# Kernel tuning notes

Hardware: AMD Instinct MI355X
Metric: run time of the kernel (lower is better)

## Reference

```python
import jax, jax.numpy as jnp
import numpy as np

B, C, H, W = 16, 256, 64, 64
NH, DH = 8, 64
POS_C = 4


def setup_inputs() -> dict:
    key = jax.random.key(0)
    ks = jax.random.split(key, 10)
    cin = C + POS_C
    dqkv = NH * DH
    sc = 1.0 / np.sqrt(cin)
    inp = {
        "x": jax.random.normal(ks[0], (B, C, H, W), dtype=jnp.float32),
        "pos_emb": jax.random.normal(ks[1], (1, POS_C, H, W), dtype=jnp.float32) / np.sqrt(C * H * W),
        "Wk": jax.random.normal(ks[2], (dqkv, cin), dtype=jnp.float32) * sc,
        "bk": jnp.zeros((dqkv,), dtype=jnp.float32),
        "Wq": jax.random.normal(ks[3], (dqkv, cin), dtype=jnp.float32) * sc,
        "bq": jnp.zeros((dqkv,), dtype=jnp.float32),
        "Wv": jax.random.normal(ks[4], (dqkv, cin), dtype=jnp.float32) * sc,
        "bv": jnp.zeros((dqkv,), dtype=jnp.float32),
        "Wo": jax.random.normal(ks[5], (C, dqkv), dtype=jnp.float32) / np.sqrt(dqkv),
        "bo": jnp.zeros((C,), dtype=jnp.float32),
    }
    return inp


def _conv1x1(w, b, x):
    # w: (out, in), x: (B, in, H, W) -> (B, out, H, W)
    return jnp.einsum('oc,bchw->bohw', w, x) + b[None, :, None, None]


def reference(x, pos_emb, Wk, bk, Wq, bq, Wv, bv, Wo, bo):
    b, c, h, w = x.shape
    xp = jnp.concatenate([x, jnp.broadcast_to(pos_emb, (b, POS_C, h, w))], axis=1)
    K = _conv1x1(Wk, bk, xp).reshape(b, NH, DH, h, w)
    Q = _conv1x1(Wq, bq, xp).reshape(b, NH, DH, h, w)
    V = _conv1x1(Wv, bv, xp).reshape(b, NH, DH, h, w)
    # Row (width-axis) logits: (B, nh, H, W, W)
    qk_w = jnp.einsum('bhdij,bhdik->bhijk', Q, K)
    # Column (height-axis) logits: (B, nh, H, W, H)
    qk_h = jnp.einsum('bhdij,bhdkj->bhijk', Q, K)
    scale = 1.0 / np.sqrt(w + h)
    p = jax.nn.softmax(jnp.concatenate([qk_w, qk_h], axis=-1) * scale, axis=-1)
    p_w, p_h = p[..., :w], p[..., w:]
    a_w = jnp.einsum('bhijk,bhdik->bhdij', p_w, V)
    a_h = jnp.einsum('bhijk,bhdkj->bhdij', p_h, V)
    A = (a_w + a_h).reshape(b, NH * DH, h, w)
    return x + _conv1x1(Wo, bo, A)
```

## Files before the change

kernel.cpp:

```cpp
#include <hip/hip_runtime.h>

typedef unsigned short u16;
typedef __bf16 bf16x8 __attribute__((ext_vector_type(8)));
typedef float f32x4 __attribute__((ext_vector_type(4)));
typedef unsigned short u16x8 __attribute__((ext_vector_type(8)));
typedef unsigned short u16x4 __attribute__((ext_vector_type(4)));

#define MFMA16(A,B,C) __builtin_amdgcn_mfma_f32_16x16x32_bf16(A,B,C,0,0,0)

__device__ __forceinline__ float b2f(u16 h){ unsigned u = ((unsigned)h)<<16; return __builtin_bit_cast(float,u); }
__device__ __forceinline__ u16 f2b(float f){ unsigned u = __builtin_bit_cast(unsigned,f); u += 0x7fffu + ((u>>16)&1u); return (u16)(u>>16); }
__device__ __forceinline__ bf16x8 ldb8(const u16* p){ return __builtin_bit_cast(bf16x8, *(const u16x8*)p); }

__device__ __forceinline__ void g2lds16(const u16* g, u16* l){
  __builtin_amdgcn_global_load_lds((const __attribute__((address_space(1))) void*)g,
                                   (__attribute__((address_space(3))) void*)l, 16, 0, 0);
}

#define BAR   __builtin_amdgcn_s_barrier()
#define LGKM0 do{ asm volatile("s_waitcnt lgkmcnt(0)" ::: "memory"); __builtin_amdgcn_sched_barrier(0); }while(0)
#define VMC4  asm volatile("s_waitcnt vmcnt(4)" ::: "memory")
#define VMC0  asm volatile("s_waitcnt vmcnt(0)" ::: "memory")


__global__ void k_prep_w(const float* __restrict__ Wq, const float* __restrict__ Wk,
                         const float* __restrict__ Wv, const float* __restrict__ bq,
                         const float* __restrict__ bk, const float* __restrict__ bv,
                         const float* __restrict__ Wo,
                         u16* __restrict__ WP, u16* __restrict__ BIAS,
                         u16* __restrict__ WoP){
  int r = blockIdx.x;
  int tid = threadIdx.x;
  if (r < 1536){
    int t = r >> 9, rm = r & 511;
    const float* src = (t==0 ? Wq : (t==1 ? Wk : Wv)) + (long)rm*260;
    WP[(long)r*320 + tid] = f2b(src[tid]);
    if (tid < 64) WP[(long)r*320 + 256 + tid] = (tid < 4) ? f2b(src[256 + tid]) : (u16)0;
    if (tid == 0){
      const float* bs = (t==0 ? bq : (t==1 ? bk : bv));
      BIAS[r] = f2b(bs[rm]);
    }
  } else {
    int co = r - 1536;
    WoP[(long)co*512 + tid]       = f2b(Wo[(long)co*512 + tid]);
    WoP[(long)co*512 + 256 + tid] = f2b(Wo[(long)co*512 + 256 + tid]);
  }
}

__global__ void k_sentinel(float* __restrict__ out){
  long i = (long)blockIdx.x*256 + threadIdx.x;
  out[i] = 100.0f;
}

__global__ __launch_bounds__(256) void k_cvtx(const float* __restrict__ x,
                                              const float* __restrict__ pos,
                                              u16* __restrict__ XT, int b0){
  __shared__ u16 tile[64*65];
  int bidx = blockIdx.x;
  int ct = bidx & 3, pt = (bidx>>2)&63, bl = bidx>>8;
  int c0 = ct*64, p0 = pt*64;
  int tid = threadIdx.x;
  const float* xb = x + (long)(b0+bl)*256*4096;
  #pragma unroll
  for (int it=0; it<16; ++it){
    int idx = it*256 + tid; int cc = idx>>6, px = idx&63;
    tile[cc*65 + px] = f2b(xb[(long)(c0+cc)*4096 + p0 + px]);
  }
  __syncthreads();
  u16* dst = XT + ((long)(bl*4096 + p0))*320 + c0;
  #pragma unroll
  for (int it=0; it<4; ++it){
    int idx = it*256 + tid; int pp = idx>>4, c4 = (idx&15)*4;
    u16x4 o;
    #pragma unroll
    for (int u=0;u<4;++u) o[u] = tile[(c4+u)*65 + pp];
    *(u16x4*)&dst[(long)pp*320 + c4] = o;
  }
  if (ct == 0){
    int px = tid>>2, cb = (tid&3)*16;
    u16* row = XT + ((long)(bl*4096 + p0 + px))*320 + 256 + cb;
    #pragma unroll
    for (int half=0; half<2; ++half){
      u16x8 o;
      #pragma unroll
      for (int u=0;u<8;++u){
        int c = cb + half*8 + u;
        o[u] = (c < 4) ? f2b(pos[(long)c*4096 + p0 + px]) : (u16)0;
      }
      *(u16x8*)&row[half*8] = o;
    }
  }
}

__global__ __launch_bounds__(512,2) void k_qkv(
    const u16* __restrict__ XT, const u16* __restrict__ WP,
    const u16* __restrict__ BIAS,
    u16* __restrict__ Qb, u16* __restrict__ Kb, u16* __restrict__ Vt, int nwg){
  __shared__ u16 sm[65536];
  int hw = blockIdx.x;
  int bidx = (hw & 7)*(nwg >> 3) + (hw >> 3);
  int mt = bidx % 6; long nt = bidx / 6;
  int oc0 = mt*256;
  int bl = (int)(nt >> 4); int pl0 = ((int)nt & 15)*256;
  int tid = threadIdx.x;
  int wid = tid>>6, lane = tid&63, l16 = lane&15, qd = lane>>4;
  int wm = wid>>2, wn = wid&3;
  const u16* gA = WP + (long)oc0*320;
  const u16* gB = XT + ((long)nt*256)*320;

  int b2=(lane>>2)&1, b3=(lane>>3)&1, b4=(lane>>4)&1;
  int lanez = lane ^ ((b2^b4) | (b3<<1) | (b4<<2));
  int srowz = lanez>>2, scolz = (lanez&3)*8;

  f32x4 zf = {0.f,0.f,0.f,0.f};
  f32x4 acc[8][4];
  #pragma unroll
  for (int i=0;i<8;++i){
    #pragma unroll
    for (int j=0;j<4;++j) acc[i][j] = zf;
  }

  auto stage2 = [&](const u16* g, int ldsOff){
    g2lds16(g + (long)(wid*16 + srowz)*320 + scolz,        &sm[ldsOff + wid*512]);
    g2lds16(g + (long)(128 + wid*16 + srowz)*320 + scolz,  &sm[ldsOff + 4096 + wid*512]);
  };
  auto aOff = [&](int buf,int ks){ return (buf*2+ks)*8192; };
  auto bOff = [&](int buf,int ks){ return 32768 + (buf*2+ks)*8192; };
  auto swz = [&](int row, int q){ int byt = (row*64 + q*16) ^ ((row&7)<<4); return byt>>1; };

  bf16x8 rA[4], rB[4];
  auto ldA4 = [&](int buf,int ks,int mh){
    int o = aOff(buf,ks);
    #pragma unroll
    for (int i=0;i<4;++i) rA[i] = ldb8(&sm[o + swz(wm*128 + mh*64 + i*16 + l16, qd)]);
  };
  auto ldB4 = [&](int buf,int ks){
    int o = bOff(buf,ks);
    #pragma unroll
    for (int i=0;i<4;++i) rB[i] = ldb8(&sm[o + swz(wn*64 + i*16 + l16, qd)]);
  };
  auto mmac = [&](int mh){
    __builtin_amdgcn_s_setprio(1);
    #pragma unroll
    for (int i=0;i<4;++i){
      #pragma unroll
      for (int j=0;j<4;++j)
        acc[mh*4+i][j] = MFMA16(rA[i], rB[j], acc[mh*4+i][j]);
    }
    __builtin_amdgcn_s_setprio(0);
  };

  stage2(gA + 0,  aOff(0,0));
  stage2(gB + 0,  bOff(0,0));
  stage2(gA + 32, aOff(0,1));
  stage2(gB + 32, bOff(0,1));
  VMC4; BAR;

  for (int t=0; t<5; ++t){
    int cur = t&1, nxt = cur^1;
    bool st = (t < 4);
    int k1 = (t+1)*64;
    ldB4(cur,0); ldA4(cur,0,0);
    if (st) stage2(gA + k1, aOff(nxt,0));
    BAR; LGKM0; mmac(0); BAR;
    ldA4(cur,0,1);
    if (st) stage2(gB + k1, bOff(nxt,0));
    BAR; LGKM0; mmac(1);
    if (st) { VMC4; } else { VMC0; }
    BAR;
    ldB4(cur,1); ldA4(cur,1,0);
    if (st) stage2(gA + k1 + 32, aOff(nxt,1));
    BAR; LGKM0; mmac(0); BAR;
    ldA4(cur,1,1);
    if (st) stage2(gB + k1 + 32, bOff(nxt,1));
    BAR; LGKM0; mmac(1);
    if (st) { VMC4; } else { VMC0; }
    BAR;
  }

  if (oc0 < 1024){
    const u16* dstb = (oc0 < 512) ? Qb : Kb;
    #pragma unroll
    for (int mi=0;mi<8;++mi){
      int oc = oc0 + wm*128 + mi*16 + qd*4;
      int ocm = oc & 511;
      int hh = ocm>>6, dd = ocm&63;
      float bv4[4];
      #pragma unroll
      for (int r=0;r<4;++r) bv4[r] = b2f(BIAS[oc + r]);
      #pragma unroll
      for (int ni=0;ni<4;++ni){
        int pl = pl0 + wn*64 + ni*16 + l16;
        u16x4 pk;
        #pragma unroll
        for (int r=0;r<4;++r) pk[r] = f2b(acc[mi][ni][r] + bv4[r]);
        *(u16x4*)&((u16*)dstb)[((long)(bl*8+hh)*4096 + pl)*64 + dd] = pk;
      }
    }
  } else {
    #pragma unroll
    for (int p=0;p<2;++p){
      if (wm == p){
        #pragma unroll
        for (int mi=0;mi<8;++mi){
          int ocl = mi*16 + qd*4;
          float bv4[4];
          #pragma unroll
          for (int r=0;r<4;++r) bv4[r] = b2f(BIAS[oc0 + p*128 + ocl + r]);
          #pragma unroll
          for (int ni=0;ni<4;++ni){
            int px = wn*64 + ni*16 + l16;
            #pragma unroll
            for (int r=0;r<4;++r) sm[(ocl+r)*264 + px] = f2b(acc[mi][ni][r] + bv4[r]);
          }
        }
      }
      BAR;
      #pragma unroll
      for (int it=0; it<8; ++it){
        int c = it*512 + tid;
        int ocr = c>>5, px8 = (c&31)*8;
        u16x8 o = *(const u16x8*)&sm[ocr*264 + px8];
        int ocm = (oc0 & 511) + p*128 + ocr;
        int hh = ocm>>6, dd = ocm&63;
        *(u16x8*)&Vt[(long)(bl*8+hh)*262144 + (long)dd*4096 + pl0 + px8] = o;
      }
      BAR;
    }
  }
}

__global__ __launch_bounds__(256) void k_vtr(const u16* __restrict__ Vt,
                                             u16* __restrict__ Vtc){
  __shared__ u16 tile[64*68];
  int bid = blockIdx.x;
  int d = bid & 63; long ph = bid >> 6;
  const u16* src = Vt + ph*262144 + (long)d*4096;
  u16* dst = Vtc + ph*262144 + (long)d*4096;
  int tid = threadIdx.x;
  #pragma unroll
  for (int it=0; it<2; ++it){
    int idx = it*256 + tid; int i = idx>>3, j8 = (idx&7)*8;
    u16x8 v = *(const u16x8*)&src[i*64 + j8];
    u16x4 lo = {v[0],v[1],v[2],v[3]}, hi = {v[4],v[5],v[6],v[7]};
    *(u16x4*)&tile[i*68 + j8]     = lo;
    *(u16x4*)&tile[i*68 + j8 + 4] = hi;
  }
  __syncthreads();
  #pragma unroll
  for (int it=0; it<2; ++it){
    int idx = it*256 + tid; int j = idx>>3, i8 = (idx&7)*8;
    u16x8 o;
    #pragma unroll
    for (int u=0;u<8;++u) o[u] = tile[(i8+u)*68 + j];
    *(u16x8*)&dst[j*64 + i8] = o;
  }
}

template<int COL>
__global__ __launch_bounds__(256) void k_attn(
    const u16* __restrict__ Qb, const u16* __restrict__ Kb,
    const u16* __restrict__ Vsrc, u16* __restrict__ U,
    float* __restrict__ M, float* __restrict__ L){
  __shared__ u16 sm[4*64*72];
  u16* Qs = sm;
  u16* Ks = sm + 4608;
  u16* VT = sm + 9216;
  u16* Ps = sm + 13824;
  int bid = blockIdx.x;
  int rc = bid&63, h=(bid>>6)&7, bl=bid>>9;
  long plane  = (long)(bl*8+h)*262144;
  long sbase  = (long)(bl*8+h)*4096;
  int tid = threadIdx.x;
  #pragma unroll
  for (int it=0; it<2; ++it){
    int idx = it*256 + tid; int row = idx>>3, c8 = (idx&7)*8;
    long gqk = plane + ((long)(COL ? (row*64 + rc) : (rc*64 + row)))*64 + c8;
    *(u16x8*)&Qs[row*72 + c8] = *(const u16x8*)&Qb[gqk];
    *(u16x8*)&Ks[row*72 + c8] = *(const u16x8*)&Kb[gqk];
    long gv = plane + (long)row*4096 + rc*64 + c8;
    *(u16x8*)&VT[row*72 + c8] = *(const u16x8*)&Vsrc[gv];
  }
  __syncthreads();
  int wid = tid>>6, lane = tid&63, l16 = lane&15, qd = lane>>4;
  int j0 = wid*16;
  f32x4 zf = {0.f,0.f,0.f,0.f};
  f32x4 sv[4] = {zf,zf,zf,zf};
  #pragma unroll
  for (int d0=0; d0<64; d0+=32){
    bf16x8 a = ldb8(&Qs[(j0+l16)*72 + d0 + qd*8]);
    #pragma unroll
    for (int n=0;n<4;++n){
      bf16x8 bb = ldb8(&Ks[(n*16+l16)*72 + d0 + qd*8]);
      sv[n] = MFMA16(a, bb, sv[n]);
    }
  }
  const float scale = 0.08838834764831845f;
  float mrow[4], lrow[4];
  #pragma unroll
  for (int r=0;r<4;++r){
    float mv = -1e30f;
    #pragma unroll
    for (int n=0;n<4;++n){ sv[n][r] *= scale; mv = fmaxf(mv, sv[n][r]); }
    mv = fmaxf(mv, __shfl_xor(mv,1)); mv = fmaxf(mv, __shfl_xor(mv,2));
    mv = fmaxf(mv, __shfl_xor(mv,4)); mv = fmaxf(mv, __shfl_xor(mv,8));
    float ls = 0.f;
    #pragma unroll
    for (int n=0;n<4;++n){ float p = expf(fminf(sv[n][r]-mv, 0.f)); sv[n][r] = p; ls += p; }
    ls += __shfl_xor(ls,1); ls += __shfl_xor(ls,2);
    ls += __shfl_xor(ls,4); ls += __shfl_xor(ls,8);
    mrow[r]=mv; lrow[r]=ls;
    int qi = j0 + qd*4 + r;
    #pragma unroll
    for (int n=0;n<4;++n) Ps[qi*72 + n*16 + l16] = f2b(sv[n][r]);
  }
  __syncthreads();
  f32x4 u4[4] = {zf,zf,zf,zf};
  #pragma unroll
  for (int k0=0;k0<64;k0+=32){
    bf16x8 a = ldb8(&Ps[(j0+l16)*72 + k0 + qd*8]);
    #pragma unroll
    for (int n=0;n<4;++n){
      bf16x8 bb = ldb8(&VT[(n*16+l16)*72 + k0 + qd*8]);
      u4[n] = MFMA16(a, bb, u4[n]);
    }
  }
  if (!COL){
    #pragma unroll
    for (int r=0;r<4;++r){
      int qi = j0 + qd*4 + r;
      long pl = (long)rc*64 + qi;
      long ob = (sbase + pl)*64;
      #pragma unroll
      for (int n=0;n<4;++n) U[ob + n*16 + l16] = f2b(u4[n][r]);
      if (l16==0){ M[sbase+pl]=mrow[r]; L[sbase+pl]=lrow[r]; }
    }
  } else {
    #pragma unroll
    for (int r=0;r<4;++r){
      int qi = j0 + qd*4 + r;
      long pix = sbase + (long)qi*64 + rc;
      float mw = M[pix], lw = L[pix];
      float mh = mrow[r], lh = lrow[r];
      float m  = fmaxf(mw, mh);
      float ew = expf(fminf(mw - m, 0.f));
      float eh = expf(fminf(mh - m, 0.f));
      float rden = 1.f / fmaxf(ew*lw + eh*lh, 1e-20f);
      long ob = pix*64;
      #pragma unroll
      for (int n=0;n<4;++n){
        float uw = b2f(U[ob + n*16 + l16]);
        U[ob + n*16 + l16] = f2b((ew*uw + eh*u4[n][r])*rden);
      }
    }
  }
}

__global__ __launch_bounds__(256) void k_oproj(
    const u16* __restrict__ WoP, const float* __restrict__ bo,
    const u16* __restrict__ AC, const float* __restrict__ x,
    float* __restrict__ out, int b0){
  __shared__ u16 sW[128*32];
  __shared__ u16 sA[128*32];
  int bidx = blockIdx.x;
  int mt = bidx & 1; long nt = bidx >> 1;
  int co0 = mt*128; long p0 = nt*128;
  int bl = (int)(p0>>12), pl0 = (int)(p0&4095);
  int gb = b0 + bl;
  int tid = threadIdx.x;
  int wid=tid>>6, lane=tid&63, l16=lane&15, qd=lane>>4;
  int wm=wid>>1, wn=wid&1;
  int srow = lane>>2, sc8 = (lane&3)*8;
  f32x4 zf = {0.f,0.f,0.f,0.f};
  f32x4 acc[4][4];
  #pragma unroll
  for (int i=0;i<4;++i){
    #pragma unroll
    for (int j=0;j<4;++j) acc[i][j] = zf;
  }
  for (int kk=0; kk<512; kk+=32){
    __syncthreads();
    #pragma unroll
    for (int c=0;c<2;++c){
      int seg = wid*2 + c;
      int row = seg*16 + srow;
      g2lds16(&WoP[(long)(co0+row)*512 + kk + sc8], &sW[seg*512]);
      g2lds16(&AC[((long)(bl*8+(kk>>6))*4096 + pl0 + row)*64 + (kk&63) + sc8], &sA[seg*512]);
    }
    __syncthreads();
    bf16x8 a[4], bb[4];
    #pragma unroll
    for (int mi=0;mi<4;++mi) a[mi]  = ldb8(&sW[(wm*64+mi*16+l16)*32 + qd*8]);
    #pragma unroll
    for (int ni=0;ni<4;++ni) bb[ni] = ldb8(&sA[(wn*64+ni*16+l16)*32 + qd*8]);
    #pragma unroll
    for (int mi=0;mi<4;++mi){
      #pragma unroll
      for (int ni=0;ni<4;++ni)
        acc[mi][ni] = MFMA16(a[mi], bb[ni], acc[mi][ni]);
    }
  }
  #pragma unroll
  for (int mi=0;mi<4;++mi){
    #pragma unroll
    for (int ni=0;ni<4;++ni){
      int n = wn*64+ni*16+l16; int pl = pl0+n;
      #pragma unroll
      for (int r=0;r<4;++r){
        int co = co0 + wm*64+mi*16+qd*4+r;
        long addr = ((long)(gb*256+co))*4096 + pl;
        out[addr] = acc[mi][ni][r] + bo[co] + x[addr];
      }
    }
  }
}

extern "C" void kernel_launch(void* const* d_in, const int* in_sizes, int n_in,
                              void* d_out, int out_size, void* d_ws, size_t ws_size,
                              hipStream_t stream) {
  (void)in_sizes; (void)n_in; (void)out_size;
  const float* x    = (const float*)d_in[0];
  const float* pos  = (const float*)d_in[1];
  const float* Wk   = (const float*)d_in[2];
  const float* bk   = (const float*)d_in[3];
  const float* Wq   = (const float*)d_in[4];
  const float* bq   = (const float*)d_in[5];
  const float* Wv   = (const float*)d_in[6];
  const float* bv   = (const float*)d_in[7];
  const float* Wo   = (const float*)d_in[8];
  const float* bo   = (const float*)d_in[9];
  float* out = (float*)d_out;
  char* ws = (char*)d_ws;

  const long per_batch = 23855104l;
  const long fixed = 1248256l;
  if (fixed + per_batch > (long)ws_size){
    k_sentinel<<<65536, 256, 0, stream>>>(out);
    return;
  }
  int CB = 16;
  while (CB > 1 && fixed + (long)CB*per_batch > (long)ws_size) CB >>= 1;

  u16*  WP   = (u16*)(ws);
  u16*  BIAS = (u16*)(ws + 983040l);
  u16*  WoP  = (u16*)(ws + 986112l);
  long base  = fixed;
  u16*  XT   = (u16*)(ws + base);
  u16*  Qc   = (u16*)(ws + base + (long)CB*2621440l);
  u16*  Kc   = (u16*)((char*)Qc  + (long)CB*4194304l);
  u16*  Vt   = (u16*)((char*)Kc  + (long)CB*4194304l);
  u16*  Vtc  = (u16*)((char*)Vt  + (long)CB*4194304l);
  u16*  Uw   = (u16*)((char*)Vtc + (long)CB*4194304l);
  float* MWc = (float*)((char*)Uw + (long)CB*4194304l);
  float* LWc = (float*)((char*)MWc + (long)CB*131072l);

  k_prep_w<<<1792, 256, 0, stream>>>(Wq, Wk, Wv, bq, bk, bv, Wo, WP, BIAS, WoP);
  for (int b0 = 0; b0 < 16; b0 += CB){
    k_cvtx    <<<CB*256, 256, 0, stream>>>(x, pos, XT, b0);
    k_qkv     <<<CB*96,  512, 0, stream>>>(XT, WP, BIAS, Qc, Kc, Vt, CB*96);
    k_vtr     <<<CB*512, 256, 0, stream>>>(Vt, Vtc);
    k_attn<0> <<<CB*512, 256, 0, stream>>>(Qc, Kc, Vt,  Uw, MWc, LWc);
    k_attn<1> <<<CB*512, 256, 0, stream>>>(Qc, Kc, Vtc, Uw, MWc, LWc);
    k_oproj   <<<CB*64,  256, 0, stream>>>(WoP, bo, Uw, x, out, b0);
  }
}
```

Before: 424.3 us.

## Store V pixel-major and transpose it in LDS inside attention, dropping k_vtr

The QKV projection now writes V in the same pixel-major layout as Q and K. Both attention passes load V with the Q/K indexing and transpose it into LDS with an XOR swizzle to limit bank conflicts. This removes the separate V transpose kernel and its extra global buffer, saving a full read and write of V and one launch. In exchange the attention kernels do scalar strided LDS writes. The QKV kernel also drops its explicit lgkmcnt waits and scheduling barriers, and relaxes its launch-bounds occupancy hint, which changes register allocation and instruction scheduling.

```diff
diff --git a/kernel.cpp b/kernel.cpp
--- a/kernel.cpp
+++ b/kernel.cpp
@@ -18,7 +18,6 @@
 }
 
 #define BAR   __builtin_amdgcn_s_barrier()
-#define LGKM0 do{ asm volatile("s_waitcnt lgkmcnt(0)" ::: "memory"); __builtin_amdgcn_sched_barrier(0); }while(0)
 #define VMC4  asm volatile("s_waitcnt vmcnt(4)" ::: "memory")
 #define VMC0  asm volatile("s_waitcnt vmcnt(0)" ::: "memory")
 
@@ -92,10 +91,10 @@
   }
 }
 
-__global__ __launch_bounds__(512,2) void k_qkv(
+__global__ __launch_bounds__(512) void k_qkv(
     const u16* __restrict__ XT, const u16* __restrict__ WP,
     const u16* __restrict__ BIAS,
-    u16* __restrict__ Qb, u16* __restrict__ Kb, u16* __restrict__ Vt, int nwg){
+    u16* __restrict__ Qb, u16* __restrict__ Kb, u16* __restrict__ Vb, int nwg){
   __shared__ u16 sm[65536];
   int hw = blockIdx.x;
   int bidx = (hw & 7)*(nwg >> 3) + (hw >> 3);
@@ -162,98 +161,39 @@
     int k1 = (t+1)*64;
     ldB4(cur,0); ldA4(cur,0,0);
     if (st) stage2(gA + k1, aOff(nxt,0));
-    BAR; LGKM0; mmac(0); BAR;
+    BAR; mmac(0); BAR;
     ldA4(cur,0,1);
     if (st) stage2(gB + k1, bOff(nxt,0));
-    BAR; LGKM0; mmac(1);
+    BAR; mmac(1);
     if (st) { VMC4; } else { VMC0; }
     BAR;
     ldB4(cur,1); ldA4(cur,1,0);
     if (st) stage2(gA + k1 + 32, aOff(nxt,1));
-    BAR; LGKM0; mmac(0); BAR;
+    BAR; mmac(0); BAR;
     ldA4(cur,1,1);
     if (st) stage2(gB + k1 + 32, bOff(nxt,1));
-    BAR; LGKM0; mmac(1);
+    BAR; mmac(1);
     if (st) { VMC4; } else { VMC0; }
     BAR;
   }
 
-  if (oc0 < 1024){
-    const u16* dstb = (oc0 < 512) ? Qb : Kb;
-    #pragma unroll
-    for (int mi=0;mi<8;++mi){
-      int oc = oc0 + wm*128 + mi*16 + qd*4;
-      int ocm = oc & 511;
-      int hh = ocm>>6, dd = ocm&63;
-      float bv4[4];
-      #pragma unroll
-      for (int r=0;r<4;++r) bv4[r] = b2f(BIAS[oc + r]);
-      #pragma unroll
-      for (int ni=0;ni<4;++ni){
-        int pl = pl0 + wn*64 + ni*16 + l16;
-        u16x4 pk;
-        #pragma unroll
-        for (int r=0;r<4;++r) pk[r] = f2b(acc[mi][ni][r] + bv4[r]);
-        *(u16x4*)&((u16*)dstb)[((long)(bl*8+hh)*4096 + pl)*64 + dd] = pk;
-      }
-    }
-  } else {
-    #pragma unroll
-    for (int p=0;p<2;++p){
-      if (wm == p){
-        #pragma unroll
-        for (int mi=0;mi<8;++mi){
-          int ocl = mi*16 + qd*4;
-          float bv4[4];
-          #pragma unroll
-          for (int r=0;r<4;++r) bv4[r] = b2f(BIAS[oc0 + p*128 + ocl + r]);
-          #pragma unroll
-          for (int ni=0;ni<4;++ni){
-            int px = wn*64 + ni*16 + l16;
-            #pragma unroll
-            for (int r=0;r<4;++r) sm[(ocl+r)*264 + px] = f2b(acc[mi][ni][r] + bv4[r]);
-          }
-        }
-      }
-      BAR;
-      #pragma unroll
-      for (int it=0; it<8; ++it){
-        int c = it*512 + tid;
-        int ocr = c>>5, px8 = (c&31)*8;
-        u16x8 o = *(const u16x8*)&sm[ocr*264 + px8];
-        int ocm = (oc0 & 511) + p*128 + ocr;
-        int hh = ocm>>6, dd = ocm&63;
-        *(u16x8*)&Vt[(long)(bl*8+hh)*262144 + (long)dd*4096 + pl0 + px8] = o;
-      }
-      BAR;
-    }
-  }
-}
-
-__global__ __launch_bounds__(256) void k_vtr(const u16* __restrict__ Vt,
-                                             u16* __restrict__ Vtc){
-  __shared__ u16 tile[64*68];
-  int bid = blockIdx.x;
-  int d = bid & 63; long ph = bid >> 6;
-  const u16* src = Vt + ph*262144 + (long)d*4096;
-  u16* dst = Vtc + ph*262144 + (long)d*4096;
-  int tid = threadIdx.x;
-  #pragma unroll
-  for (int it=0; it<2; ++it){
-    int idx = it*256 + tid; int i = idx>>3, j8 = (idx&7)*8;
-    u16x8 v = *(const u16x8*)&src[i*64 + j8];
-    u16x4 lo = {v[0],v[1],v[2],v[3]}, hi = {v[4],v[5],v[6],v[7]};
-    *(u16x4*)&tile[i*68 + j8]     = lo;
-    *(u16x4*)&tile[i*68 + j8 + 4] = hi;
-  }
-  __syncthreads();
-  #pragma unroll
-  for (int it=0; it<2; ++it){
-    int idx = it*256 + tid; int j = idx>>3, i8 = (idx&7)*8;
-    u16x8 o;
-    #pragma unroll
-    for (int u=0;u<8;++u) o[u] = tile[(i8+u)*68 + j];
-    *(u16x8*)&dst[j*64 + i8] = o;
+  u16* dstb = (oc0 < 512) ? Qb : (oc0 < 1024 ? Kb : Vb);
+  #pragma unroll
+  for (int mi=0;mi<8;++mi){
+    int oc = oc0 + wm*128 + mi*16 + qd*4;
+    int ocm = oc & 511;
+    int hh = ocm>>6, dd = ocm&63;
+    float bv4[4];
+    #pragma unroll
+    for (int r=0;r<4;++r) bv4[r] = b2f(BIAS[oc + r]);
+    #pragma unroll
+    for (int ni=0;ni<4;++ni){
+      int pl = pl0 + wn*64 + ni*16 + l16;
+      u16x4 pk;
+      #pragma unroll
+      for (int r=0;r<4;++r) pk[r] = f2b(acc[mi][ni][r] + bv4[r]);
+      *(u16x4*)&dstb[((long)(bl*8+hh)*4096 + pl)*64 + dd] = pk;
+    }
   }
 }
 
@@ -278,8 +218,10 @@
     long gqk = plane + ((long)(COL ? (row*64 + rc) : (rc*64 + row)))*64 + c8;
     *(u16x8*)&Qs[row*72 + c8] = *(const u16x8*)&Qb[gqk];
     *(u16x8*)&Ks[row*72 + c8] = *(const u16x8*)&Kb[gqk];
-    long gv = plane + (long)row*4096 + rc*64 + c8;
-    *(u16x8*)&VT[row*72 + c8] = *(const u16x8*)&Vsrc[gv];
+    u16x8 v = *(const u16x8*)&Vsrc[gqk];
+    int xr = row ^ ((idx&7)<<3);
+    #pragma unroll
+    for (int u=0;u<8;++u) VT[(c8+u)*72 + xr] = v[u];
   }
   __syncthreads();
   int wid = tid>>6, lane = tid&63, l16 = lane&15, qd = lane>>4;
@@ -321,7 +263,8 @@
     bf16x8 a = ldb8(&Ps[(j0+l16)*72 + k0 + qd*8]);
     #pragma unroll
     for (int n=0;n<4;++n){
-      bf16x8 bb = ldb8(&VT[(n*16+l16)*72 + k0 + qd*8]);
+      int dd = n*16 + l16;
+      bf16x8 bb = ldb8(&VT[dd*72 + ((k0 + qd*8) ^ (((dd>>3)&7)<<3))]);
       u4[n] = MFMA16(a, bb, u4[n]);
     }
   }
@@ -432,7 +375,7 @@
   float* out = (float*)d_out;
   char* ws = (char*)d_ws;
 
-  const long per_batch = 23855104l;
+  const long per_batch = 19660800l;
   const long fixed = 1248256l;
   if (fixed + per_batch > (long)ws_size){
     k_sentinel<<<65536, 256, 0, stream>>>(out);
@@ -448,19 +391,17 @@
   u16*  XT   = (u16*)(ws + base);
   u16*  Qc   = (u16*)(ws + base + (long)CB*2621440l);
   u16*  Kc   = (u16*)((char*)Qc  + (long)CB*4194304l);
-  u16*  Vt   = (u16*)((char*)Kc  + (long)CB*4194304l);
-  u16*  Vtc  = (u16*)((char*)Vt  + (long)CB*4194304l);
-  u16*  Uw   = (u16*)((char*)Vtc + (long)CB*4194304l);
+  u16*  Vc   = (u16*)((char*)Kc  + (long)CB*4194304l);
+  u16*  Uw   = (u16*)((char*)Vc  + (long)CB*4194304l);
   float* MWc = (float*)((char*)Uw + (long)CB*4194304l);
   float* LWc = (float*)((char*)MWc + (long)CB*131072l);
 
   k_prep_w<<<1792, 256, 0, stream>>>(Wq, Wk, Wv, bq, bk, bv, Wo, WP, BIAS, WoP);
   for (int b0 = 0; b0 < 16; b0 += CB){
     k_cvtx    <<<CB*256, 256, 0, stream>>>(x, pos, XT, b0);
-    k_qkv     <<<CB*96,  512, 0, stream>>>(XT, WP, BIAS, Qc, Kc, Vt, CB*96);
-    k_vtr     <<<CB*512, 256, 0, stream>>>(Vt, Vtc);
-    k_attn<0> <<<CB*512, 256, 0, stream>>>(Qc, Kc, Vt,  Uw, MWc, LWc);
-    k_attn<1> <<<CB*512, 256, 0, stream>>>(Qc, Kc, Vtc, Uw, MWc, LWc);
+    k_qkv     <<<CB*96,  512, 0, stream>>>(XT, WP, BIAS, Qc, Kc, Vc, CB*96);
+    k_attn<0> <<<CB*512, 256, 0, stream>>>(Qc, Kc, Vc, Uw, MWc, LWc);
+    k_attn<1> <<<CB*512, 256, 0, stream>>>(Qc, Kc, Vc, Uw, MWc, LWc);
     k_oproj   <<<CB*64,  256, 0, stream>>>(WoP, bo, Uw, x, out, b0);
   }
 }
```

New measurement: 407.1 us. 4.1% less time.
